# Kernel tuning notes

Hardware: AMD Instinct MI355X
Metric: run time of the kernel (lower is better)

The kernel has to match this reference:

```python
import jax, jax.numpy as jnp
import numpy as np

N = 50000
E = 800000
IN_C, HID_C, OUT_C = 128, 128, 64


def setup_inputs() -> dict:
    key = jax.random.key(0)
    ks = jax.random.split(key, 12)
    x = jax.random.normal(ks[0], (N, IN_C), dtype=jnp.float32)
    edge_index = jax.random.randint(ks[1], (2, E), 0, N, dtype=jnp.int64)
    dims = [(IN_C, HID_C), (HID_C, HID_C), (HID_C, OUT_C)]
    params = {}
    for i, (din, dout) in enumerate(dims):
        s = 1.0 / np.sqrt(din)
        params[f"Wl{i}"] = jax.random.uniform(ks[2 + 3 * i], (din, dout), jnp.float32, -s, s)
        params[f"b{i}"] = jnp.zeros((dout,), jnp.float32)
        params[f"Wr{i}"] = jax.random.uniform(ks[3 + 3 * i], (din, dout), jnp.float32, -s, s)
    return {"x": x, "edge_index": edge_index, **params}


def _sage_conv(x, src, dst, Wl, b, Wr):
    # mean-aggregate neighbor features: messages flow src -> dst
    agg = jax.ops.segment_sum(x[src], dst, num_segments=N)          # [N, d]
    deg = jax.ops.segment_sum(jnp.ones((src.shape[0],), x.dtype), dst, num_segments=N)
    agg = agg / jnp.maximum(deg, 1.0)[:, None]                      # mean (0 for isolated nodes)
    return agg @ Wl + b + x @ Wr


def reference(x, edge_index, Wl0, b0, Wr0, Wl1, b1, Wr1, Wl2, b2, Wr2):
    src, dst = edge_index[0], edge_index[1]
    h = _sage_conv(x, src, dst, Wl0, b0, Wr0)
    h = jax.nn.relu(h)  # dropout is identity in eval mode
    h = _sage_conv(h, src, dst, Wl1, b1, Wr1)
    h = jax.nn.relu(h)
    h = _sage_conv(h, src, dst, Wl2, b2, Wr2)
    return h
```

## Files before the change

kernel.cpp:

```cpp
#include <hip/hip_runtime.h>

#define N_NODES 50000
#define N_EDGES 800000
#define NBUCK 196
#define NHIST 196

typedef __attribute__((ext_vector_type(8))) short short8;
typedef __attribute__((ext_vector_type(4))) float f32x4;
typedef __attribute__((ext_vector_type(4))) unsigned short ushort4v;
typedef __attribute__((ext_vector_type(8))) unsigned short ushort8v;


__device__ inline void split_bf16(float f, unsigned short& hi, unsigned short& lo) {
    union { float f; unsigned u; } a; a.f = f;
    unsigned r = (a.u + 0x7fffu + ((a.u >> 16) & 1u)) >> 16;
    hi = (unsigned short)r;
    union { unsigned u; float f; } b; b.u = r << 16;
    union { float f; unsigned u; } c; c.f = f - b.f;
    unsigned r2 = (c.u + 0x7fffu + ((c.u >> 16) & 1u)) >> 16;
    lo = (unsigned short)r2;
}

__device__ inline unsigned short f2bf(float f) {
    union { float f; unsigned u; } a; a.f = f;
    return (unsigned short)((a.u + 0x7fffu + ((a.u >> 16) & 1u)) >> 16);
}

__device__ inline float bf2f(unsigned short u) {
    union { unsigned u; float f; } a; a.u = (unsigned)u << 16; return a.f;
}


__global__ void prep_kernel(const float* __restrict__ W0, const float* __restrict__ W1,
                            const float* __restrict__ W2, const float* __restrict__ W3,
                            const float* __restrict__ W4, const float* __restrict__ W5,
                            unsigned short* __restrict__ wout,
                            const float* __restrict__ x, unsigned short* __restrict__ xhi,
                            unsigned short* __restrict__ xlo,
                            const int* __restrict__ dst, int* __restrict__ blkhist) {
    __shared__ int lhist[NBUCK];
    if (blockIdx.x < 320) {
        int t = blockIdx.x * 256 + threadIdx.x;
        const float* W; int D, local, half; size_t base;
        if (t < 65536) {
            int mat = t >> 14; local = t & 16383; D = 128; half = 16384;
            base = (size_t)mat * 32768;
            W = mat == 0 ? W0 : mat == 1 ? W1 : mat == 2 ? W2 : W3;
        } else {
            int m = (t - 65536) >> 13; local = (t - 65536) & 8191; D = 64; half = 8192;
            base = 131072 + (size_t)m * 16384;
            W = m == 0 ? W4 : W5;
        }
        int j = local & 7, lane = (local >> 3) & 63, ks = (local >> 9) & 3, ct = local >> 11;
        int k = ks * 32 + ((lane >> 4) << 3) + j;
        int n = (ct << 4) + (lane & 15);
        unsigned short hi, lo;
        split_bf16(W[k * D + n], hi, lo);
        wout[base + local] = hi;
        wout[base + half + local] = lo;
    } else if (blockIdx.x < 1883) {
        int t = (blockIdx.x - 320) * 256 + threadIdx.x;
        if (t >= N_NODES * 8) return;
        const float* p = x + (size_t)t * 16;
#pragma unroll
        for (int half = 0; half < 2; ++half) {
            float4 v0 = *(const float4*)(p + half * 8);
            float4 v1 = *(const float4*)(p + half * 8 + 4);
            float vv[8] = {v0.x, v0.y, v0.z, v0.w, v1.x, v1.y, v1.z, v1.w};
            ushort8v h, l;
#pragma unroll
            for (int j = 0; j < 8; ++j) {
                unsigned short a, b;
                split_bf16(vv[j], a, b);
                h[j] = a; l[j] = b;
            }
            *(ushort8v*)(xhi + (size_t)t * 16 + half * 8) = h;
            *(ushort8v*)(xlo + (size_t)t * 16 + half * 8) = l;
        }
    } else {
        const int hb = blockIdx.x - 1883;
        const int base = hb * 4096;
        if (threadIdx.x < NBUCK) lhist[threadIdx.x] = 0;
        __syncthreads();
#pragma unroll
        for (int i = 0; i < 16; ++i) {
            int e = base + i * 256 + threadIdx.x;
            if (e < N_EDGES) atomicAdd(&lhist[dst[e] >> 8], 1);
        }
        __syncthreads();
        if (threadIdx.x < NBUCK) blkhist[hb * NBUCK + threadIdx.x] = lhist[threadIdx.x];
    }
}


__global__ void scan_sums_kernel(const int* __restrict__ blkhist,
                                 int* __restrict__ bucketBase, int* __restrict__ bucketCur,
                                 int* __restrict__ rowptr) {
    __shared__ int s[256];
    int tid = threadIdx.x;
    int v = 0;
    if (tid < NBUCK)
        for (int h = 0; h < NHIST; ++h) v += blkhist[h * NBUCK + tid];
    s[tid] = v;
    __syncthreads();
    for (int off = 1; off < 256; off <<= 1) {
        int t = (tid >= off) ? s[tid - off] : 0;
        __syncthreads();
        s[tid] += t;
        __syncthreads();
    }
    if (tid < NBUCK) {
        int b = s[tid] - v;
        bucketBase[tid] = b;
        bucketCur[tid] = b;
    }
    if (tid == 0) { bucketBase[NBUCK] = N_EDGES; rowptr[N_NODES] = N_EDGES; }
}


__global__ __launch_bounds__(256) void partition_kernel(
    const int* __restrict__ src, const int* __restrict__ dst,
    int* __restrict__ bucketCur, unsigned int* __restrict__ ebuf, int E) {
    __shared__ int hist[NBUCK], binoff[NBUCK], bincur[NBUCK], runstart[NBUCK];
    __shared__ int scanbuf[256];
    __shared__ unsigned int sortbuf[2048];
    const int tid = threadIdx.x;
    const int base = blockIdx.x * 2048;
    if (tid < NBUCK) hist[tid] = 0;
    __syncthreads();
    int myb[8]; unsigned int myp[8];
#pragma unroll
    for (int i = 0; i < 8; ++i) {
        int e = base + i * 256 + tid;
        if (e < E) {
            int d = dst[e], s = src[e];
            myb[i] = d >> 8;
            myp[i] = ((unsigned)d << 16) | (unsigned)s;
            atomicAdd(&hist[myb[i]], 1);
        } else myb[i] = -1;
    }
    __syncthreads();
    int v = (tid < NBUCK) ? hist[tid] : 0;
    scanbuf[tid] = v;
    __syncthreads();
    for (int off = 1; off < 256; off <<= 1) {
        int t = (tid >= off) ? scanbuf[tid - off] : 0;
        __syncthreads();
        scanbuf[tid] += t;
        __syncthreads();
    }
    if (tid < NBUCK) {
        binoff[tid] = scanbuf[tid] - v;
        bincur[tid] = 0;
        runstart[tid] = atomicAdd(&bucketCur[tid], v);
    }
    __syncthreads();
#pragma unroll
    for (int i = 0; i < 8; ++i) {
        if (myb[i] >= 0) {
            int r = atomicAdd(&bincur[myb[i]], 1);
            sortbuf[binoff[myb[i]] + r] = myp[i];
        }
    }
    __syncthreads();
    int nloc = E - base; if (nloc > 2048) nloc = 2048;
#pragma unroll
    for (int i = 0; i < 8; ++i) {
        int idx = i * 256 + tid;
        if (idx < nloc) {
            unsigned int p = sortbuf[idx];
            int b = p >> 24;
            ebuf[runstart[b] + (idx - binoff[b])] = p;
        }
    }
}


__global__ __launch_bounds__(256) void fine_fill_kernel(
    const unsigned int* __restrict__ ebuf, const int* __restrict__ bucketBase,
    int* __restrict__ rowptr, unsigned short* __restrict__ esrc, int n) {
    __shared__ int cnt[256], scanbuf[256], cur[256];
    const int b = blockIdx.x, tid = threadIdx.x;
    const int nbase = b << 8;
    cnt[tid] = 0;
    __syncthreads();
    const int lo = bucketBase[b], hi = bucketBase[b + 1];
    for (int k = lo + tid; k < hi; k += 256)
        atomicAdd(&cnt[(ebuf[k] >> 16) & 255], 1);
    __syncthreads();
    int v = cnt[tid];
    scanbuf[tid] = v;
    __syncthreads();
    for (int off = 1; off < 256; off <<= 1) {
        int t = (tid >= off) ? scanbuf[tid - off] : 0;
        __syncthreads();
        scanbuf[tid] += t;
        __syncthreads();
    }
    int start = lo + scanbuf[tid] - v;
    if (nbase + tid < n) rowptr[nbase + tid] = start;
    cur[tid] = start;
    __syncthreads();
    for (int k = lo + tid; k < hi; k += 256) {
        unsigned int p = ebuf[k];
        int pos = atomicAdd(&cur[(p >> 16) & 255], 1);
        esrc[pos] = (unsigned short)(p & 0xFFFFu);
    }
}


__global__ __launch_bounds__(256, 8) void agg_kernel(
    const unsigned short* __restrict__ Hhi, const int* __restrict__ rowptr,
    const unsigned short* __restrict__ esrc,
    unsigned short* __restrict__ Ahi, int n) {
    int g = (blockIdx.x * blockDim.x + threadIdx.x) >> 4;
    int l16 = threadIdx.x & 15;
    if (g >= n) return;
    int beg = rowptr[g], end = rowptr[g + 1];
    const unsigned short* __restrict__ Hb = Hhi + l16 * 8;
    float a0[8] = {0,0,0,0,0,0,0,0}, a1[8] = {0,0,0,0,0,0,0,0};
    int k = beg;
    for (; k + 6 <= end; k += 6) {
        int e0 = esrc[k],     e1 = esrc[k + 1], e2 = esrc[k + 2];
        int e3 = esrc[k + 3], e4 = esrc[k + 4], e5 = esrc[k + 5];
        ushort8v v0 = *(const ushort8v*)(Hb + (size_t)e0 * 128);
        ushort8v v1 = *(const ushort8v*)(Hb + (size_t)e1 * 128);
        ushort8v v2 = *(const ushort8v*)(Hb + (size_t)e2 * 128);
        ushort8v v3 = *(const ushort8v*)(Hb + (size_t)e3 * 128);
        ushort8v v4 = *(const ushort8v*)(Hb + (size_t)e4 * 128);
        ushort8v v5 = *(const ushort8v*)(Hb + (size_t)e5 * 128);
#pragma unroll
        for (int j = 0; j < 8; ++j) {
            a0[j] += bf2f(v0[j]); a1[j] += bf2f(v1[j]);
            a0[j] += bf2f(v2[j]); a1[j] += bf2f(v3[j]);
            a0[j] += bf2f(v4[j]); a1[j] += bf2f(v5[j]);
        }
    }
    for (; k + 2 <= end; k += 2) {
        int e0 = esrc[k], e1 = esrc[k + 1];
        ushort8v v0 = *(const ushort8v*)(Hb + (size_t)e0 * 128);
        ushort8v v1 = *(const ushort8v*)(Hb + (size_t)e1 * 128);
#pragma unroll
        for (int j = 0; j < 8; ++j) { a0[j] += bf2f(v0[j]); a1[j] += bf2f(v1[j]); }
    }
    if (k < end) {
        int e0 = esrc[k];
        ushort8v v0 = *(const ushort8v*)(Hb + (size_t)e0 * 128);
#pragma unroll
        for (int j = 0; j < 8; ++j) a0[j] += bf2f(v0[j]);
    }
    float inv = (end > beg) ? 1.0f / (float)(end - beg) : 0.0f;
    ushort8v mh;
#pragma unroll
    for (int j = 0; j < 8; ++j) mh[j] = f2bf((a0[j] + a1[j]) * inv);
    *(ushort8v*)(Ahi + (size_t)g * 128 + l16 * 8) = mh;
}


template <int DOUT, bool RELU, bool SPLIT_OUT>
__global__ __launch_bounds__(256, 4) void gemm_planes(
    const unsigned short* __restrict__ A1hi,
    const unsigned short* __restrict__ A2hi, const unsigned short* __restrict__ A2lo,
    const unsigned short* __restrict__ B1p, const unsigned short* __restrict__ B2p,
    const float* __restrict__ bias, float* __restrict__ outf,
    unsigned short* __restrict__ outhi, unsigned short* __restrict__ outlo, int M) {
    constexpr int K = 128, BM = 32, KS = 4, CT = DOUT / 16, CPW = CT / 4;
    constexpr int PITCH = K + 8;
    constexpr int HALF = CT * KS * 512;
    __shared__ unsigned short As[3][BM * PITCH];

    const int tid = threadIdx.x;
    const int r0 = blockIdx.x * BM;

    const unsigned short* __restrict__ srcs[3] = {A1hi, A2hi, A2lo};
#pragma unroll
    for (int s = 0; s < 3; ++s) {
#pragma unroll
        for (int c = 0; c < 2; ++c) {
            int chunk = tid + c * 256;
            int row = chunk >> 4;
            int c8 = (chunk & 15) * 8;
            int grow = r0 + row; if (grow >= M) grow = M - 1;
            *(ushort8v*)(&As[s][row * PITCH + c8]) =
                *(const ushort8v*)(srcs[s] + (size_t)grow * K + c8);
        }
    }
    __syncthreads();

    const int wave = tid >> 6, lane = tid & 63;
    const int rl = lane & 15, quad = lane >> 4;

    f32x4 acc[2][CPW];
#pragma unroll
    for (int c = 0; c < CPW; ++c) {
        float bv = bias[(wave * CPW + c) * 16 + rl];
        acc[0][c] = (f32x4){bv, bv, bv, bv};
        acc[1][c] = acc[0][c];
    }

#pragma unroll
    for (int ks = 0; ks < KS; ++ks) {
        short8 a_ag[2], a_sh[2][2];
#pragma unroll
        for (int rt = 0; rt < 2; ++rt) {
            int off = (rt * 16 + rl) * PITCH + ks * 32 + quad * 8;
            a_ag[rt]    = *(const short8*)(&As[0][off]);
            a_sh[rt][0] = *(const short8*)(&As[1][off]);
            a_sh[rt][1] = *(const short8*)(&As[2][off]);
        }
        short8 b1[CPW][2], b2[CPW][2];
#pragma unroll
        for (int c = 0; c < CPW; ++c) {
            size_t boff = (((wave * CPW + c) * KS + ks) * 64 + lane) * 8;
#pragma unroll
            for (int p = 0; p < 2; ++p) {
                b1[c][p] = *(const short8*)(B1p + p * HALF + boff);
                b2[c][p] = *(const short8*)(B2p + p * HALF + boff);
            }
        }
#pragma unroll
        for (int rt = 0; rt < 2; ++rt)
#pragma unroll
            for (int c = 0; c < CPW; ++c) {
                acc[rt][c] = __builtin_amdgcn_mfma_f32_16x16x32_bf16(a_ag[rt],    b1[c][0], acc[rt][c], 0, 0, 0);
                acc[rt][c] = __builtin_amdgcn_mfma_f32_16x16x32_bf16(a_ag[rt],    b1[c][1], acc[rt][c], 0, 0, 0);
                acc[rt][c] = __builtin_amdgcn_mfma_f32_16x16x32_bf16(a_sh[rt][0], b2[c][0], acc[rt][c], 0, 0, 0);
                acc[rt][c] = __builtin_amdgcn_mfma_f32_16x16x32_bf16(a_sh[rt][0], b2[c][1], acc[rt][c], 0, 0, 0);
                acc[rt][c] = __builtin_amdgcn_mfma_f32_16x16x32_bf16(a_sh[rt][1], b2[c][0], acc[rt][c], 0, 0, 0);
            }
    }

#pragma unroll
    for (int rt = 0; rt < 2; ++rt)
#pragma unroll
        for (int c = 0; c < CPW; ++c) {
            int col = (wave * CPW + c) * 16 + rl;
            int rowb = r0 + rt * 16 + quad * 4;
#pragma unroll
            for (int r = 0; r < 4; ++r) {
                int rr = rowb + r;
                if (rr < M) {
                    float vv = acc[rt][c][r];
                    if (RELU) vv = fmaxf(vv, 0.f);
                    if (SPLIT_OUT) {
                        unsigned short h, l;
                        split_bf16(vv, h, l);
                        outhi[(size_t)rr * DOUT + col] = h;
                        outlo[(size_t)rr * DOUT + col] = l;
                    } else {
                        outf[(size_t)rr * DOUT + col] = vv;
                    }
                }
            }
        }
}


extern "C" void kernel_launch(void* const* d_in, const int* in_sizes, int n_in,
                              void* d_out, int out_size, void* d_ws, size_t ws_size,
                              hipStream_t stream) {
    const float* x   = (const float*)d_in[0];
    const int* eidx  = (const int*)d_in[1];
    const int* src   = eidx;
    const int* dst   = eidx + N_EDGES;
    const float* Wl0 = (const float*)d_in[2];
    const float* b0  = (const float*)d_in[3];
    const float* Wr0 = (const float*)d_in[4];
    const float* Wl1 = (const float*)d_in[5];
    const float* b1  = (const float*)d_in[6];
    const float* Wr1 = (const float*)d_in[7];
    const float* Wl2 = (const float*)d_in[8];
    const float* b2  = (const float*)d_in[9];
    const float* Wr2 = (const float*)d_in[10];
    float* outp = (float*)d_out;

    unsigned short* xhi  = (unsigned short*)d_ws;
    unsigned short* xlo  = xhi + (size_t)N_NODES * 128;
    unsigned short* aghi = xlo + (size_t)N_NODES * 128;
    unsigned int* ebuf = (unsigned int*)aghi;
    int* rowptr    = (int*)(aghi + (size_t)N_NODES * 128);
    int* blkhist   = rowptr + 50016;
    int* bucketBase= blkhist + 38416;
    int* bucketCur = bucketBase + 256;
    unsigned short* esrc  = (unsigned short*)(bucketCur + 256);
    unsigned short* packw = esrc + N_EDGES;
    unsigned short* Wl0p = packw;
    unsigned short* Wr0p = packw + 32768;
    unsigned short* Wl1p = packw + 65536;
    unsigned short* Wr1p = packw + 98304;
    unsigned short* Wl2p = packw + 131072;
    unsigned short* Wr2p = packw + 147456;

    prep_kernel<<<2079, 256, 0, stream>>>(Wl0, Wr0, Wl1, Wr1, Wl2, Wr2, packw,
                                          x, xhi, xlo, dst, blkhist);
    scan_sums_kernel<<<1, 256, 0, stream>>>(blkhist, bucketBase, bucketCur, rowptr);
    partition_kernel<<<(N_EDGES + 2047) / 2048, 256, 0, stream>>>(src, dst, bucketCur, ebuf, N_EDGES);
    fine_fill_kernel<<<NBUCK, 256, 0, stream>>>(ebuf, bucketBase, rowptr, esrc, N_NODES);

    const int aggGrid = (N_NODES * 16 + 255) / 256;
    const int gemmGrid = (N_NODES + 31) / 32;

    agg_kernel<<<aggGrid, 256, 0, stream>>>(xhi, rowptr, esrc, aghi, N_NODES);
    gemm_planes<128, true, true><<<gemmGrid, 256, 0, stream>>>(
        aghi, xhi, xlo, Wl0p, Wr0p, b0, nullptr, xhi, xlo, N_NODES);
    agg_kernel<<<aggGrid, 256, 0, stream>>>(xhi, rowptr, esrc, aghi, N_NODES);
    gemm_planes<128, true, true><<<gemmGrid, 256, 0, stream>>>(
        aghi, xhi, xlo, Wl1p, Wr1p, b1, nullptr, xhi, xlo, N_NODES);
    agg_kernel<<<aggGrid, 256, 0, stream>>>(xhi, rowptr, esrc, aghi, N_NODES);
    gemm_planes<64, false, false><<<gemmGrid, 256, 0, stream>>>(
        aghi, xhi, xlo, Wl2p, Wr2p, b2, outp, nullptr, nullptr, N_NODES);
}
```

Baseline: 270.5 us.

## Quantize node features to int8 with per-row scale for neighbor aggregation

Adds a per-row int8 quantized copy of node features, with a max-abs scale, produced in prep and in the GEMM epilogue. The aggregation kernel then gathers 8 bytes per lane instead of 16, which halves the bytes of the random neighbor gathers, and dequantizes by accumulating value*scale and subtracting a 128*sum(scale) offset. The cost is an extra row-max reduction with a block sync and an extra int8 write per GEMM, plus a large drop in precision of the aggregated features that may break tolerance.

Result: no change. 267.7 us (-1.1%).

```diff
diff --git a/kernel.cpp b/kernel.cpp
--- a/kernel.cpp
+++ b/kernel.cpp
@@ -7,8 +7,8 @@
 
 typedef __attribute__((ext_vector_type(8))) short short8;
 typedef __attribute__((ext_vector_type(4))) float f32x4;
-typedef __attribute__((ext_vector_type(4))) unsigned short ushort4v;
 typedef __attribute__((ext_vector_type(8))) unsigned short ushort8v;
+typedef __attribute__((ext_vector_type(16))) unsigned char uchar16;
 
 
 __device__ inline void split_bf16(float f, unsigned short& hi, unsigned short& lo) {
@@ -30,6 +30,20 @@
     union { unsigned u; float f; } a; a.u = (unsigned)u << 16; return a.f;
 }
 
+__device__ inline unsigned char q8(float v, float qs) {
+    int qi = (int)rintf(v * qs);
+    qi = qi > 127 ? 127 : (qi < -127 ? -127 : qi);
+    return (unsigned char)(qi + 128);
+}
+
+__device__ inline void acc8(float* a, uint2 w, float s) {
+#pragma unroll
+    for (int j = 0; j < 4; ++j) {
+        a[j]     += (float)((w.x >> (8 * j)) & 255u) * s;
+        a[j + 4] += (float)((w.y >> (8 * j)) & 255u) * s;
+    }
+}
+
 
 __global__ void prep_kernel(const float* __restrict__ W0, const float* __restrict__ W1,
                             const float* __restrict__ W2, const float* __restrict__ W3,
@@ -37,6 +51,7 @@
                             unsigned short* __restrict__ wout,
                             const float* __restrict__ x, unsigned short* __restrict__ xhi,
                             unsigned short* __restrict__ xlo,
+                            unsigned char* __restrict__ xq, float* __restrict__ xsc,
                             const int* __restrict__ dst, int* __restrict__ blkhist) {
     __shared__ int lhist[NBUCK];
     if (blockIdx.x < 320) {
@@ -62,21 +77,34 @@
         int t = (blockIdx.x - 320) * 256 + threadIdx.x;
         if (t >= N_NODES * 8) return;
         const float* p = x + (size_t)t * 16;
-#pragma unroll
-        for (int half = 0; half < 2; ++half) {
-            float4 v0 = *(const float4*)(p + half * 8);
-            float4 v1 = *(const float4*)(p + half * 8 + 4);
-            float vv[8] = {v0.x, v0.y, v0.z, v0.w, v1.x, v1.y, v1.z, v1.w};
-            ushort8v h, l;
-#pragma unroll
-            for (int j = 0; j < 8; ++j) {
-                unsigned short a, b;
-                split_bf16(vv[j], a, b);
-                h[j] = a; l[j] = b;
-            }
-            *(ushort8v*)(xhi + (size_t)t * 16 + half * 8) = h;
-            *(ushort8v*)(xlo + (size_t)t * 16 + half * 8) = l;
-        }
+        float4 v0 = *(const float4*)(p);
+        float4 v1 = *(const float4*)(p + 4);
+        float4 v2 = *(const float4*)(p + 8);
+        float4 v3 = *(const float4*)(p + 12);
+        float vv[16] = {v0.x, v0.y, v0.z, v0.w, v1.x, v1.y, v1.z, v1.w,
+                        v2.x, v2.y, v2.z, v2.w, v3.x, v3.y, v3.z, v3.w};
+        float m = 0.f;
+#pragma unroll
+        for (int j = 0; j < 16; ++j) m = fmaxf(m, fabsf(vv[j]));
+        m = fmaxf(m, __shfl_xor(m, 1));
+        m = fmaxf(m, __shfl_xor(m, 2));
+        m = fmaxf(m, __shfl_xor(m, 4));
+        float qs = m > 0.f ? 127.0f / m : 0.0f;
+        uchar16 qv;
+        ushort8v h0, l0, h1, l1;
+#pragma unroll
+        for (int j = 0; j < 16; ++j) {
+            unsigned short a, b;
+            split_bf16(vv[j], a, b);
+            if (j < 8) { h0[j] = a; l0[j] = b; } else { h1[j - 8] = a; l1[j - 8] = b; }
+            qv[j] = q8(vv[j], qs);
+        }
+        *(ushort8v*)(xhi + (size_t)t * 16) = h0;
+        *(ushort8v*)(xhi + (size_t)t * 16 + 8) = h1;
+        *(ushort8v*)(xlo + (size_t)t * 16) = l0;
+        *(ushort8v*)(xlo + (size_t)t * 16 + 8) = l1;
+        *(uchar16*)(xq + (size_t)t * 16) = qv;
+        if ((t & 7) == 0) xsc[t >> 3] = m * (1.0f / 127.0f);
     } else {
         const int hb = blockIdx.x - 1883;
         const int base = hb * 4096;
@@ -210,49 +238,52 @@
 
 
 __global__ __launch_bounds__(256, 8) void agg_kernel(
-    const unsigned short* __restrict__ Hhi, const int* __restrict__ rowptr,
-    const unsigned short* __restrict__ esrc,
+    const unsigned char* __restrict__ Hq, const float* __restrict__ Hsc,
+    const int* __restrict__ rowptr, const unsigned short* __restrict__ esrc,
     unsigned short* __restrict__ Ahi, int n) {
     int g = (blockIdx.x * blockDim.x + threadIdx.x) >> 4;
     int l16 = threadIdx.x & 15;
     if (g >= n) return;
     int beg = rowptr[g], end = rowptr[g + 1];
-    const unsigned short* __restrict__ Hb = Hhi + l16 * 8;
+    const unsigned char* __restrict__ Hb = Hq + l16 * 8;
     float a0[8] = {0,0,0,0,0,0,0,0}, a1[8] = {0,0,0,0,0,0,0,0};
+    float sacc = 0.f;
     int k = beg;
     for (; k + 6 <= end; k += 6) {
         int e0 = esrc[k],     e1 = esrc[k + 1], e2 = esrc[k + 2];
         int e3 = esrc[k + 3], e4 = esrc[k + 4], e5 = esrc[k + 5];
-        ushort8v v0 = *(const ushort8v*)(Hb + (size_t)e0 * 128);
-        ushort8v v1 = *(const ushort8v*)(Hb + (size_t)e1 * 128);
-        ushort8v v2 = *(const ushort8v*)(Hb + (size_t)e2 * 128);
-        ushort8v v3 = *(const ushort8v*)(Hb + (size_t)e3 * 128);
-        ushort8v v4 = *(const ushort8v*)(Hb + (size_t)e4 * 128);
-        ushort8v v5 = *(const ushort8v*)(Hb + (size_t)e5 * 128);
-#pragma unroll
-        for (int j = 0; j < 8; ++j) {
-            a0[j] += bf2f(v0[j]); a1[j] += bf2f(v1[j]);
-            a0[j] += bf2f(v2[j]); a1[j] += bf2f(v3[j]);
-            a0[j] += bf2f(v4[j]); a1[j] += bf2f(v5[j]);
-        }
+        uint2 w0 = *(const uint2*)(Hb + (size_t)e0 * 128);
+        uint2 w1 = *(const uint2*)(Hb + (size_t)e1 * 128);
+        uint2 w2 = *(const uint2*)(Hb + (size_t)e2 * 128);
+        uint2 w3 = *(const uint2*)(Hb + (size_t)e3 * 128);
+        uint2 w4 = *(const uint2*)(Hb + (size_t)e4 * 128);
+        uint2 w5 = *(const uint2*)(Hb + (size_t)e5 * 128);
+        float s0 = Hsc[e0], s1 = Hsc[e1], s2 = Hsc[e2];
+        float s3 = Hsc[e3], s4 = Hsc[e4], s5 = Hsc[e5];
+        acc8(a0, w0, s0); acc8(a1, w1, s1); acc8(a0, w2, s2);
+        acc8(a1, w3, s3); acc8(a0, w4, s4); acc8(a1, w5, s5);
+        sacc += s0 + s1 + s2 + s3 + s4 + s5;
     }
     for (; k + 2 <= end; k += 2) {
         int e0 = esrc[k], e1 = esrc[k + 1];
-        ushort8v v0 = *(const ushort8v*)(Hb + (size_t)e0 * 128);
-        ushort8v v1 = *(const ushort8v*)(Hb + (size_t)e1 * 128);
-#pragma unroll
-        for (int j = 0; j < 8; ++j) { a0[j] += bf2f(v0[j]); a1[j] += bf2f(v1[j]); }
+        uint2 w0 = *(const uint2*)(Hb + (size_t)e0 * 128);
+        uint2 w1 = *(const uint2*)(Hb + (size_t)e1 * 128);
+        float s0 = Hsc[e0], s1 = Hsc[e1];
+        acc8(a0, w0, s0); acc8(a1, w1, s1);
+        sacc += s0 + s1;
     }
     if (k < end) {
         int e0 = esrc[k];
-        ushort8v v0 = *(const ushort8v*)(Hb + (size_t)e0 * 128);
-#pragma unroll
-        for (int j = 0; j < 8; ++j) a0[j] += bf2f(v0[j]);
+        uint2 w0 = *(const uint2*)(Hb + (size_t)e0 * 128);
+        float s0 = Hsc[e0];
+        acc8(a0, w0, s0);
+        sacc += s0;
     }
     float inv = (end > beg) ? 1.0f / (float)(end - beg) : 0.0f;
     ushort8v mh;
 #pragma unroll
-    for (int j = 0; j < 8; ++j) mh[j] = f2bf((a0[j] + a1[j]) * inv);
+    for (int j = 0; j < 8; ++j)
+        mh[j] = f2bf((a0[j] + a1[j] - 128.0f * sacc) * inv);
     *(ushort8v*)(Ahi + (size_t)g * 128 + l16 * 8) = mh;
 }
 
@@ -263,11 +294,13 @@
     const unsigned short* __restrict__ A2hi, const unsigned short* __restrict__ A2lo,
     const unsigned short* __restrict__ B1p, const unsigned short* __restrict__ B2p,
     const float* __restrict__ bias, float* __restrict__ outf,
-    unsigned short* __restrict__ outhi, unsigned short* __restrict__ outlo, int M) {
+    unsigned short* __restrict__ outhi, unsigned short* __restrict__ outlo,
+    unsigned char* __restrict__ outq, float* __restrict__ outsc, int M) {
     constexpr int K = 128, BM = 32, KS = 4, CT = DOUT / 16, CPW = CT / 4;
     constexpr int PITCH = K + 8;
     constexpr int HALF = CT * KS * 512;
     __shared__ unsigned short As[3][BM * PITCH];
+    __shared__ float wmax[BM][4];
 
     const int tid = threadIdx.x;
     const int r0 = blockIdx.x * BM;
@@ -330,6 +363,58 @@
             }
     }
 
+    if (RELU) {
+#pragma unroll
+        for (int rt = 0; rt < 2; ++rt)
+#pragma unroll
+            for (int c = 0; c < CPW; ++c)
+#pragma unroll
+                for (int r = 0; r < 4; ++r)
+                    acc[rt][c][r] = fmaxf(acc[rt][c][r], 0.f);
+    }
+
+    float qsc[2][4];
+    if constexpr (SPLIT_OUT) {
+        float lm[2][4];
+#pragma unroll
+        for (int rt = 0; rt < 2; ++rt)
+#pragma unroll
+            for (int r = 0; r < 4; ++r) {
+                float m = fabsf(acc[rt][0][r]);
+#pragma unroll
+                for (int c = 1; c < CPW; ++c) m = fmaxf(m, fabsf(acc[rt][c][r]));
+                lm[rt][r] = m;
+            }
+#pragma unroll
+        for (int off = 1; off < 16; off <<= 1)
+#pragma unroll
+            for (int rt = 0; rt < 2; ++rt)
+#pragma unroll
+                for (int r = 0; r < 4; ++r)
+                    lm[rt][r] = fmaxf(lm[rt][r], __shfl_xor(lm[rt][r], off));
+        if (rl == 0) {
+#pragma unroll
+            for (int rt = 0; rt < 2; ++rt)
+#pragma unroll
+                for (int r = 0; r < 4; ++r)
+                    wmax[rt * 16 + quad * 4 + r][wave] = lm[rt][r];
+        }
+        __syncthreads();
+#pragma unroll
+        for (int rt = 0; rt < 2; ++rt)
+#pragma unroll
+            for (int r = 0; r < 4; ++r) {
+                int row = rt * 16 + quad * 4 + r;
+                float rm = fmaxf(fmaxf(wmax[row][0], wmax[row][1]),
+                                 fmaxf(wmax[row][2], wmax[row][3]));
+                qsc[rt][r] = rm > 0.f ? 127.0f / rm : 0.0f;
+                if (wave == 0 && rl == 0) {
+                    int rr = r0 + row;
+                    if (rr < M) outsc[rr] = rm * (1.0f / 127.0f);
+                }
+            }
+    }
+
 #pragma unroll
     for (int rt = 0; rt < 2; ++rt)
 #pragma unroll
@@ -341,12 +426,12 @@
                 int rr = rowb + r;
                 if (rr < M) {
                     float vv = acc[rt][c][r];
-                    if (RELU) vv = fmaxf(vv, 0.f);
                     if (SPLIT_OUT) {
                         unsigned short h, l;
                         split_bf16(vv, h, l);
                         outhi[(size_t)rr * DOUT + col] = h;
                         outlo[(size_t)rr * DOUT + col] = l;
+                        outq[(size_t)rr * DOUT + col] = q8(vv, qsc[rt][r]);
                     } else {
                         outf[(size_t)rr * DOUT + col] = vv;
                     }
@@ -390,9 +475,11 @@
     unsigned short* Wr1p = packw + 98304;
     unsigned short* Wl2p = packw + 131072;
     unsigned short* Wr2p = packw + 147456;
+    unsigned char* xq = (unsigned char*)(packw + 163840);
+    float* xsc = (float*)(xq + (size_t)N_NODES * 128);
 
     prep_kernel<<<2079, 256, 0, stream>>>(Wl0, Wr0, Wl1, Wr1, Wl2, Wr2, packw,
-                                          x, xhi, xlo, dst, blkhist);
+                                          x, xhi, xlo, xq, xsc, dst, blkhist);
     scan_sums_kernel<<<1, 256, 0, stream>>>(blkhist, bucketBase, bucketCur, rowptr);
     partition_kernel<<<(N_EDGES + 2047) / 2048, 256, 0, stream>>>(src, dst, bucketCur, ebuf, N_EDGES);
     fine_fill_kernel<<<NBUCK, 256, 0, stream>>>(ebuf, bucketBase, rowptr, esrc, N_NODES);
@@ -400,13 +487,13 @@
     const int aggGrid = (N_NODES * 16 + 255) / 256;
     const int gemmGrid = (N_NODES + 31) / 32;
 
-    agg_kernel<<<aggGrid, 256, 0, stream>>>(xhi, rowptr, esrc, aghi, N_NODES);
+    agg_kernel<<<aggGrid, 256, 0, stream>>>(xq, xsc, rowptr, esrc, aghi, N_NODES);
     gemm_planes<128, true, true><<<gemmGrid, 256, 0, stream>>>(
-        aghi, xhi, xlo, Wl0p, Wr0p, b0, nullptr, xhi, xlo, N_NODES);
-    agg_kernel<<<aggGrid, 256, 0, stream>>>(xhi, rowptr, esrc, aghi, N_NODES);
+        aghi, xhi, xlo, Wl0p, Wr0p, b0, nullptr, xhi, xlo, xq, xsc, N_NODES);
+    agg_kernel<<<aggGrid, 256, 0, stream>>>(xq, xsc, rowptr, esrc, aghi, N_NODES);
     gemm_planes<128, true, true><<<gemmGrid, 256, 0, stream>>>(
-        aghi, xhi, xlo, Wl1p, Wr1p, b1, nullptr, xhi, xlo, N_NODES);
-    agg_kernel<<<aggGrid, 256, 0, stream>>>(xhi, rowptr, esrc, aghi, N_NODES);
+        aghi, xhi, xlo, Wl1p, Wr1p, b1, nullptr, xhi, xlo, xq, xsc, N_NODES);
+    agg_kernel<<<aggGrid, 256, 0, stream>>>(xq, xsc, rowptr, esrc, aghi, N_NODES);
     gemm_planes<64, false, false><<<gemmGrid, 256, 0, stream>>>(
-        aghi, xhi, xlo, Wl2p, Wr2p, b2, outp, nullptr, nullptr, N_NODES);
-}
+        aghi, xhi, xlo, Wl2p, Wr2p, b2, outp, nullptr, nullptr, nullptr, nullptr, N_NODES);
+}
```
